# Kernel tuning notes

Measured on AMD Instinct MI355X. Metric: run time of the kernel, lower is better.

The kernel has to match this reference:

```python
import jax, jax.numpy as jnp
import numpy as np

N_NODES = 100000
N_EDGES = 1600000


def setup_inputs() -> dict:
    key = jax.random.key(0)
    ks = jax.random.split(key, 12)
    s = lambda d: 1.0 / np.sqrt(d)
    inp = {
        "x": jax.random.normal(ks[0], (N_NODES, 64), dtype=jnp.float32),
        "edge_index": jax.random.randint(ks[1], (2, N_EDGES), 0, N_NODES, dtype=jnp.int64),
        "W_embed": jax.random.normal(ks[2], (64, 128), dtype=jnp.float32) * s(64),
        "eps1": jnp.zeros((), jnp.float32),
        "w1a": jax.random.normal(ks[3], (128, 128), dtype=jnp.float32) * s(128),
        "b1a": jnp.zeros((128,), jnp.float32),
        "w1b": jax.random.normal(ks[4], (128, 128), dtype=jnp.float32) * s(128),
        "b1b": jnp.zeros((128,), jnp.float32),
        "eps2": jnp.zeros((), jnp.float32),
        "w2a": jax.random.normal(ks[5], (128, 256), dtype=jnp.float32) * s(128),
        "b2a": jnp.zeros((256,), jnp.float32),
        "w2b": jax.random.normal(ks[6], (256, 128), dtype=jnp.float32) * s(256),
        "b2b": jnp.zeros((128,), jnp.float32),
        "eps3": jnp.zeros((), jnp.float32),
        "w3a": jax.random.normal(ks[7], (128, 256), dtype=jnp.float32) * s(128),
        "b3a": jnp.zeros((256,), jnp.float32),
        "w3b": jax.random.normal(ks[8], (256, 128), dtype=jnp.float32) * s(256),
        "b3b": jnp.zeros((128,), jnp.float32),
    }
    return inp


def _aggregate(h, src, dst, n):
    # GINConv sum aggregation: out[i] = sum_{(j,i) in E} h[j]
    return jax.ops.segment_sum(h[src], dst, num_segments=n)


def reference(x, edge_index, W_embed, eps1, w1a, b1a, w1b, b1b,
              eps2, w2a, b2a, w2b, b2b, eps3, w3a, b3a, w3b, b3b):
    src, dst = edge_index[0], edge_index[1]
    n = x.shape[0]
    # node_attr_encoder: linear embedding (dropout p=0 -> identity)
    h = x @ W_embed  # [N, dim]
    # conv1: nn((1+eps)*h + sum_neighbors), nn = Lin->ReLU->Lin
    z = (1.0 + eps1) * h + _aggregate(h, src, dst, n)
    h = jax.nn.relu(z @ w1a + b1a) @ w1b + b1b
    # conv2/conv3: nn = Lin->ReLU->Lin->ReLU
    z = (1.0 + eps2) * h + _aggregate(h, src, dst, n)
    h = jax.nn.relu(jax.nn.relu(z @ w2a + b2a) @ w2b + b2b)
    z = (1.0 + eps3) * h + _aggregate(h, src, dst, n)
    h = jax.nn.relu(jax.nn.relu(z @ w3a + b3a) @ w3b + b3b)
    return h
```

## Files before the change

### kernel.cpp

```cpp
#include <hip/hip_runtime.h>
#include <hip/hip_bf16.h>
#include <stdint.h>


typedef __attribute__((ext_vector_type(8))) short short8;
typedef __attribute__((ext_vector_type(16))) float float16v;
typedef __attribute__((ext_vector_type(4))) unsigned int uint4v;

#define BKT 512
#define NBMAX 256

#define MFMA32 __builtin_amdgcn_mfma_f32_32x32x16_bf16

union U4S8 { uint4v u; short8 s; };

__device__ __forceinline__ float b2f_lo(unsigned int u) {
    return __uint_as_float(u << 16);
}
__device__ __forceinline__ float b2f_hi(unsigned int u) {
    return __uint_as_float(u & 0xffff0000u);
}
__device__ __forceinline__ unsigned short f2b(float f) {
    unsigned int u = __float_as_uint(f);
    return (unsigned short)((u + 0x7fffu + ((u >> 16) & 1u)) >> 16);
}
__device__ __forceinline__ unsigned cvtpk_bf16(float a, float b) {
    unsigned r;
    asm("v_cvt_pk_bf16_f32 %0, %1, %2" : "=v"(r) : "v"(a), "v"(b));
    return r;
}
__device__ __forceinline__ void perm32swap(unsigned& a, unsigned& b) {
    asm("v_permlane32_swap_b32 %0, %1" : "+v"(a), "+v"(b));
}

__global__ void detect_i64_kernel(const unsigned int* ei, int* flag) {
    if (threadIdx.x == 0) {
        int is64 = 1;
        for (int e = 0; e < 64; ++e)
            if (ei[2 * e + 1] != 0u) { is64 = 0; break; }
        *flag = is64;
    }
}

__device__ __forceinline__ int edge_at(const int* ei32, int is64, long long pos) {
    if (is64) return (int)(((const long long*)ei32)[pos]);
    return ei32[pos];
}

__global__ __launch_bounds__(256) void part_hist_kernel(
        const int* __restrict__ ei, const int* __restrict__ flag,
        int* __restrict__ bh, int E, int NB, int PB) {
    __shared__ int h[NBMAX];
    const int g = blockIdx.x, tid = threadIdx.x;
    const int is64 = *flag;
    for (int i = tid; i < NB; i += 256) h[i] = 0;
    __syncthreads();
    const int e0 = g * PB, e1 = min(e0 + PB, E);
    for (int e = e0 + tid; e < e1; e += 256) {
        int d = edge_at(ei, is64, (long long)E + e);
        atomicAdd(&h[d >> 9], 1);
    }
    __syncthreads();
    for (int i = tid; i < NB; i += 256) bh[i * gridDim.x + g] = h[i];
}

__global__ __launch_bounds__(1024) void scan1_kernel(
        const int* __restrict__ in, int* __restrict__ out,
        int* __restrict__ partial, int n) {
    __shared__ int sm[1024];
    const int t = threadIdx.x;
    const int i = blockIdx.x * 1024 + t;
    int v = (i < n) ? in[i] : 0;
    sm[t] = v;
    __syncthreads();
#pragma unroll
    for (int off = 1; off < 1024; off <<= 1) {
        int x = (t >= off) ? sm[t - off] : 0;
        __syncthreads();
        sm[t] += x;
        __syncthreads();
    }
    if (i < n) out[i] = sm[t] - v;
    if (t == 1023) partial[blockIdx.x] = sm[1023];
}

__global__ __launch_bounds__(256) void scan2_kernel(
        int* __restrict__ partial, int* __restrict__ blockoff, int g1) {
    __shared__ int sm[256];
    const int t = threadIdx.x;
    int v = (t < g1) ? partial[t] : 0;
    sm[t] = v;
    __syncthreads();
#pragma unroll
    for (int off = 1; off < 256; off <<= 1) {
        int x = (t >= off) ? sm[t - off] : 0;
        __syncthreads();
        sm[t] += x;
        __syncthreads();
    }
    blockoff[t] = sm[t] - v;
}

__global__ __launch_bounds__(1024) void scan3g_kernel(
        int* __restrict__ a, const int* __restrict__ blockoff, int n) {
    int i = blockIdx.x * 1024 + threadIdx.x;
    if (i < n) a[i] += blockoff[blockIdx.x];
}

__global__ __launch_bounds__(256) void part_scatter_kernel(
        const int* __restrict__ ei, const int* __restrict__ flag,
        const int* __restrict__ bhs, unsigned int* __restrict__ staged,
        int E, int NB, int PB) {
    __shared__ int cur[NBMAX];
    const int g = blockIdx.x, tid = threadIdx.x;
    const int is64 = *flag;
    for (int i = tid; i < NB; i += 256) cur[i] = bhs[i * gridDim.x + g];
    __syncthreads();
    const int e0 = g * PB, e1 = min(e0 + PB, E);
    for (int e = e0 + tid; e < e1; e += 256) {
        int d = edge_at(ei, is64, (long long)E + e);
        int s = edge_at(ei, is64, (long long)e);
        int b = d >> 9;
        int p = atomicAdd(&cur[b], 1);
        staged[p] = ((unsigned int)(d & (BKT - 1)) << 17) | (unsigned int)s;
    }
}

__global__ __launch_bounds__(256) void csr_local_kernel(
        const unsigned int* __restrict__ staged, const int* __restrict__ bhs,
        int* __restrict__ offs, int* __restrict__ csr, int N, int E, int NB, int G2) {
    __shared__ int hist[BKT];
    __shared__ int cur[BKT];
    const int b = blockIdx.x;
    const int tid = threadIdx.x;
    const int start = bhs[b * G2];
    const int end = (b + 1 < NB) ? bhs[(b + 1) * G2] : E;
    const int node0 = b * BKT;
    for (int i = tid; i < BKT; i += 256) hist[i] = 0;
    __syncthreads();
    for (int i = start + tid; i < end; i += 256)
        atomicAdd(&hist[staged[i] >> 17], 1);
    __syncthreads();
    const int i0 = tid * 2, i1 = i0 + 1;
    for (int off = 1; off < BKT; off <<= 1) {
        int v0 = (i0 >= off) ? hist[i0 - off] : 0;
        int v1 = (i1 >= off) ? hist[i1 - off] : 0;
        __syncthreads();
        hist[i0] += v0;
        hist[i1] += v1;
        __syncthreads();
    }
    for (int i = tid; i < BKT; i += 256) {
        int node = node0 + i;
        if (node < N) {
            int e0 = start + ((i == 0) ? 0 : hist[i - 1]);
            offs[node] = e0;
            cur[i] = e0;
        }
    }
    if (b == NB - 1 && tid == 0) offs[N] = E;
    __syncthreads();
    for (int i = start + tid; i < end; i += 256) {
        unsigned int v = staged[i];
        int dl = v >> 17;
        int src = (int)(v & 0x1ffff);
        int p = atomicAdd(&cur[dl], 1);
        csr[p] = src;
    }
}

struct PW { const float* W; unsigned short* o; int K; int KOUT; };
struct PWAll { PW d[7]; int cum[8]; };

__global__ __launch_bounds__(256) void packall_kernel(PWAll P) {
    int id = blockIdx.x * blockDim.x + threadIdx.x;
    if (id >= P.cum[7]) return;
    int w = 0;
#pragma unroll
    for (int k = 1; k < 7; ++k) w += (id >= P.cum[k]);
    const int local = id - P.cum[w];
    const float* W = P.d[w].W;
    unsigned short* out = P.d[w].o;
    const int K = P.d[w].K, KOUT = P.d[w].KOUT;
    const int KS = K / 16;
    const int l = local & 63;
    const int s = (local >> 6) % KS;
    const int T = local / (KS * 64);
    const int kbase = s * 16 + ((l >> 5) << 3);
    const int n = T * 32 + (l & 31);
#pragma unroll
    for (int j = 0; j < 8; ++j)
        out[(long long)local * 8 + j] = f2b(W[(long long)(kbase + j) * KOUT + n]);
}

__global__ __launch_bounds__(256) void mm_embed(
        const float* __restrict__ X, const unsigned short* __restrict__ Wp,
        unsigned short* __restrict__ out, int Mreal) {
    constexpr int KS = 4;
    const int tid = threadIdx.x;
    const int w = tid >> 6;
    const int l = tid & 63;
    const int lm = l & 31;
    const int lk = l >> 5;
    const int wr = w & 1, wc = w >> 1;
    const long long R0 = (long long)blockIdx.x * 128 + wr * 64;
    const int T0 = (wc * 64) >> 5;

    const long long r0 = (R0 + lm < Mreal) ? (R0 + lm) : (Mreal - 1);
    const long long r1 = (R0 + 32 + lm < Mreal) ? (R0 + 32 + lm) : (Mreal - 1);
    const float* xr0 = X + r0 * 64 + lk * 8;
    const float* xr1 = X + r1 * 64 + lk * 8;
    const unsigned short* bb0 = Wp + ((long long)T0 * KS * 64 + l) * 8;
    const unsigned short* bb1 = Wp + ((long long)(T0 + 1) * KS * 64 + l) * 8;

    float16v acc00 = {}, acc01 = {}, acc10 = {}, acc11 = {};
#pragma unroll
    for (int s = 0; s < KS; ++s) {
        float4 f0a = *(const float4*)(xr0 + s * 16);
        float4 f0b = *(const float4*)(xr0 + s * 16 + 4);
        float4 f1a = *(const float4*)(xr1 + s * 16);
        float4 f1b = *(const float4*)(xr1 + s * 16 + 4);
        short8 a0, a1;
        a0[0] = (short)f2b(f0a.x); a0[1] = (short)f2b(f0a.y);
        a0[2] = (short)f2b(f0a.z); a0[3] = (short)f2b(f0a.w);
        a0[4] = (short)f2b(f0b.x); a0[5] = (short)f2b(f0b.y);
        a0[6] = (short)f2b(f0b.z); a0[7] = (short)f2b(f0b.w);
        a1[0] = (short)f2b(f1a.x); a1[1] = (short)f2b(f1a.y);
        a1[2] = (short)f2b(f1a.z); a1[3] = (short)f2b(f1a.w);
        a1[4] = (short)f2b(f1b.x); a1[5] = (short)f2b(f1b.y);
        a1[6] = (short)f2b(f1b.z); a1[7] = (short)f2b(f1b.w);
        short8 b0 = *(const short8*)(bb0 + (long long)s * 64 * 8);
        short8 b1 = *(const short8*)(bb1 + (long long)s * 64 * 8);
        acc00 = MFMA32(a0, b0, acc00, 0, 0, 0);
        acc01 = MFMA32(a0, b1, acc01, 0, 0, 0);
        acc10 = MFMA32(a1, b0, acc10, 0, 0, 0);
        acc11 = MFMA32(a1, b1, acc11, 0, 0, 0);
    }
    auto st = [&](float16v acc, long long rb, int col) {
#pragma unroll
        for (int r = 0; r < 16; ++r) {
            long long row = rb + (r & 3) + 8 * (r >> 2);
            out[row * 128 + col] = f2b(acc[r]);
        }
    };
    const long long rbase = R0 + 4 * lk;
    st(acc00, rbase,      wc * 64 + lm);
    st(acc01, rbase,      wc * 64 + 32 + lm);
    st(acc10, rbase + 32, wc * 64 + lm);
    st(acc11, rbase + 32, wc * 64 + 32 + lm);
}

__global__ __launch_bounds__(256) void aggz_kernel(
        const unsigned short* __restrict__ H, const int* __restrict__ offs,
        const int* __restrict__ csr, const float* __restrict__ eps,
        unsigned short* __restrict__ Z, int n) {
    const int node = blockIdx.x * 16 + (threadIdx.x >> 4);
    const int c8 = (threadIdx.x & 15) << 3;
    const int lane = threadIdx.x & 63;
    const int bpb = (lane & 48) << 2;
    const int g16 = threadIdx.x & 15;
    if (node >= n) return;
    const int beg = offs[node];
    const int end = offs[node + 1];
    const unsigned short* Hc = H + c8;
    const uint4 uh = *(const uint4*)(Hc + ((long long)node << 7));
    float a0 = 0.f, a1 = 0.f, a2 = 0.f, a3 = 0.f;
    float a4 = 0.f, a5 = 0.f, a6 = 0.f, a7 = 0.f;
    int i = beg;
    for (; i + 8 <= end; i += 8) {
        const int myidx = csr[i + (g16 & 7)];
        const int s0 = __builtin_amdgcn_ds_bpermute(bpb + 0,  myidx);
        const int s1 = __builtin_amdgcn_ds_bpermute(bpb + 4,  myidx);
        const int s2 = __builtin_amdgcn_ds_bpermute(bpb + 8,  myidx);
        const int s3 = __builtin_amdgcn_ds_bpermute(bpb + 12, myidx);
        const int s4 = __builtin_amdgcn_ds_bpermute(bpb + 16, myidx);
        const int s5 = __builtin_amdgcn_ds_bpermute(bpb + 20, myidx);
        const int s6 = __builtin_amdgcn_ds_bpermute(bpb + 24, myidx);
        const int s7 = __builtin_amdgcn_ds_bpermute(bpb + 28, myidx);
        const uint4 u0 = *(const uint4*)(Hc + ((long long)s0 << 7));
        const uint4 u1 = *(const uint4*)(Hc + ((long long)s1 << 7));
        const uint4 u2 = *(const uint4*)(Hc + ((long long)s2 << 7));
        const uint4 u3 = *(const uint4*)(Hc + ((long long)s3 << 7));
        const uint4 u4 = *(const uint4*)(Hc + ((long long)s4 << 7));
        const uint4 u5 = *(const uint4*)(Hc + ((long long)s5 << 7));
        const uint4 u6 = *(const uint4*)(Hc + ((long long)s6 << 7));
        const uint4 u7 = *(const uint4*)(Hc + ((long long)s7 << 7));
        a0 += ((b2f_lo(u0.x) + b2f_lo(u1.x)) + (b2f_lo(u2.x) + b2f_lo(u3.x)))
            + ((b2f_lo(u4.x) + b2f_lo(u5.x)) + (b2f_lo(u6.x) + b2f_lo(u7.x)));
        a1 += ((b2f_hi(u0.x) + b2f_hi(u1.x)) + (b2f_hi(u2.x) + b2f_hi(u3.x)))
            + ((b2f_hi(u4.x) + b2f_hi(u5.x)) + (b2f_hi(u6.x) + b2f_hi(u7.x)));
        a2 += ((b2f_lo(u0.y) + b2f_lo(u1.y)) + (b2f_lo(u2.y) + b2f_lo(u3.y)))
            + ((b2f_lo(u4.y) + b2f_lo(u5.y)) + (b2f_lo(u6.y) + b2f_lo(u7.y)));
        a3 += ((b2f_hi(u0.y) + b2f_hi(u1.y)) + (b2f_hi(u2.y) + b2f_hi(u3.y)))
            + ((b2f_hi(u4.y) + b2f_hi(u5.y)) + (b2f_hi(u6.y) + b2f_hi(u7.y)));
        a4 += ((b2f_lo(u0.z) + b2f_lo(u1.z)) + (b2f_lo(u2.z) + b2f_lo(u3.z)))
            + ((b2f_lo(u4.z) + b2f_lo(u5.z)) + (b2f_lo(u6.z) + b2f_lo(u7.z)));
        a5 += ((b2f_hi(u0.z) + b2f_hi(u1.z)) + (b2f_hi(u2.z) + b2f_hi(u3.z)))
            + ((b2f_hi(u4.z) + b2f_hi(u5.z)) + (b2f_hi(u6.z) + b2f_hi(u7.z)));
        a6 += ((b2f_lo(u0.w) + b2f_lo(u1.w)) + (b2f_lo(u2.w) + b2f_lo(u3.w)))
            + ((b2f_lo(u4.w) + b2f_lo(u5.w)) + (b2f_lo(u6.w) + b2f_lo(u7.w)));
        a7 += ((b2f_hi(u0.w) + b2f_hi(u1.w)) + (b2f_hi(u2.w) + b2f_hi(u3.w)))
            + ((b2f_hi(u4.w) + b2f_hi(u5.w)) + (b2f_hi(u6.w) + b2f_hi(u7.w)));
    }
    for (; i + 3 < end; i += 4) {
        const int j0 = csr[i], j1 = csr[i + 1], j2 = csr[i + 2], j3 = csr[i + 3];
        const uint4 u0 = *(const uint4*)(Hc + ((long long)j0 << 7));
        const uint4 u1 = *(const uint4*)(Hc + ((long long)j1 << 7));
        const uint4 u2 = *(const uint4*)(Hc + ((long long)j2 << 7));
        const uint4 u3 = *(const uint4*)(Hc + ((long long)j3 << 7));
        a0 += (b2f_lo(u0.x) + b2f_lo(u1.x)) + (b2f_lo(u2.x) + b2f_lo(u3.x));
        a1 += (b2f_hi(u0.x) + b2f_hi(u1.x)) + (b2f_hi(u2.x) + b2f_hi(u3.x));
        a2 += (b2f_lo(u0.y) + b2f_lo(u1.y)) + (b2f_lo(u2.y) + b2f_lo(u3.y));
        a3 += (b2f_hi(u0.y) + b2f_hi(u1.y)) + (b2f_hi(u2.y) + b2f_hi(u3.y));
        a4 += (b2f_lo(u0.z) + b2f_lo(u1.z)) + (b2f_lo(u2.z) + b2f_lo(u3.z));
        a5 += (b2f_hi(u0.z) + b2f_hi(u1.z)) + (b2f_hi(u2.z) + b2f_hi(u3.z));
        a6 += (b2f_lo(u0.w) + b2f_lo(u1.w)) + (b2f_lo(u2.w) + b2f_lo(u3.w));
        a7 += (b2f_hi(u0.w) + b2f_hi(u1.w)) + (b2f_hi(u2.w) + b2f_hi(u3.w));
    }
    for (; i < end; ++i) {
        const uint4 u0 = *(const uint4*)(Hc + ((long long)csr[i] << 7));
        a0 += b2f_lo(u0.x); a1 += b2f_hi(u0.x);
        a2 += b2f_lo(u0.y); a3 += b2f_hi(u0.y);
        a4 += b2f_lo(u0.z); a5 += b2f_hi(u0.z);
        a6 += b2f_lo(u0.w); a7 += b2f_hi(u0.w);
    }
    const float e = 1.0f + eps[0];
    a0 = fmaf(e, b2f_lo(uh.x), a0); a1 = fmaf(e, b2f_hi(uh.x), a1);
    a2 = fmaf(e, b2f_lo(uh.y), a2); a3 = fmaf(e, b2f_hi(uh.y), a3);
    a4 = fmaf(e, b2f_lo(uh.z), a4); a5 = fmaf(e, b2f_hi(uh.z), a5);
    a6 = fmaf(e, b2f_lo(uh.w), a6); a7 = fmaf(e, b2f_hi(uh.w), a7);
    uint4 o;
    o.x = ((unsigned int)f2b(a1) << 16) | (unsigned int)f2b(a0);
    o.y = ((unsigned int)f2b(a3) << 16) | (unsigned int)f2b(a2);
    o.z = ((unsigned int)f2b(a5) << 16) | (unsigned int)f2b(a4);
    o.w = ((unsigned int)f2b(a7) << 16) | (unsigned int)f2b(a6);
    *(uint4*)(Z + ((long long)node << 7) + c8) = o;
}


#define CVT_TO_PA2(ACC, P0, P1) do {                                   \
        unsigned X1 = cvtpk_bf16((ACC)[0], (ACC)[1]);                  \
        unsigned Y1 = cvtpk_bf16((ACC)[4], (ACC)[5]);                  \
        unsigned X2 = cvtpk_bf16((ACC)[2], (ACC)[3]);                  \
        unsigned Y2 = cvtpk_bf16((ACC)[6], (ACC)[7]);                  \
        perm32swap(X1, Y1); perm32swap(X2, Y2);                        \
        U4S8 u0; u0.u[0] = X1; u0.u[1] = X2; u0.u[2] = Y1; u0.u[3] = Y2; \
        (P0) = u0.s;                                                   \
        unsigned X3 = cvtpk_bf16((ACC)[8], (ACC)[9]);                  \
        unsigned Y3 = cvtpk_bf16((ACC)[12], (ACC)[13]);                \
        unsigned X4 = cvtpk_bf16((ACC)[10], (ACC)[11]);                \
        unsigned Y4 = cvtpk_bf16((ACC)[14], (ACC)[15]);                \
        perm32swap(X3, Y3); perm32swap(X4, Y4);                        \
        U4S8 u1; u1.u[0] = X3; u1.u[1] = X4; u1.u[2] = Y3; u1.u[3] = Y4; \
        (P1) = u1.s;                                                   \
    } while (0)

template<int KMID, bool RELU2, bool OUTF32>
__global__ __launch_bounds__(512, 2) void fused_mlp3(
        const unsigned short* __restrict__ Zin,
        const unsigned short* __restrict__ Wap, const float* __restrict__ ba,
        const unsigned short* __restrict__ Wbp, const float* __restrict__ bb,
        void* __restrict__ outp, int Mreal, int nstrips) {
    constexpr int NF = KMID / 32;
    constexpr int NCH = KMID / 16;
    constexpr int WAS = 128 * KMID;
    __shared__ unsigned short wlds[KMID * 256];
    __shared__ float blds[KMID + 128];
    const int tid = threadIdx.x;

    {
        const uint4* sa = (const uint4*)Wap;
        const uint4* sb = (const uint4*)Wbp;
        uint4* da = (uint4*)wlds;
        uint4* db = (uint4*)(wlds + WAS);
#pragma unroll
        for (int i = tid; i < KMID * 16; i += 512) { da[i] = sa[i]; db[i] = sb[i]; }
        for (int i = tid; i < KMID; i += 512) blds[i] = ba[i];
        if (tid < 128) blds[KMID + tid] = bb[tid];
    }
    __syncthreads();

    const int wid = tid >> 6;
    const int l = tid & 63;
    const int lo = l & 31;
    const int hi = l >> 5;
    const int stride = gridDim.x * 8;
    int strip = blockIdx.x * 8 + wid;
    if (strip >= nstrips) return;

    auto zload = [&](int s_, short8* zz) {
        long long zr = (long long)s_ * 32 + lo;
        if (zr >= Mreal) zr = Mreal - 1;
        const unsigned short* zrow = Zin + zr * 128 + hi * 8;
#pragma unroll
        for (int s = 0; s < 8; ++s) zz[s] = *(const short8*)(zrow + s * 16);
    };

    short8 zc[8];
    zload(strip, zc);

    while (strip < nstrips) {
        const int nxt = strip + stride;
        float16v acc2[4] = {};
        short8 zn[8];

#pragma unroll
        for (int fp = 0; fp < NF / 2; ++fp) {
            if (fp == NF / 2 - 1) {
                if (nxt < nstrips) zload(nxt, zn);
            }
            const int f0 = 2 * fp, f1 = f0 + 1;
            float16v accA, accB;
#pragma unroll
            for (int q = 0; q < 4; ++q) {
                const float4 tA = *(const float4*)(blds + f0 * 32 + q * 8 + hi * 4);
                const float4 tB = *(const float4*)(blds + f1 * 32 + q * 8 + hi * 4);
                accA[4 * q + 0] = tA.x; accA[4 * q + 1] = tA.y;
                accA[4 * q + 2] = tA.z; accA[4 * q + 3] = tA.w;
                accB[4 * q + 0] = tB.x; accB[4 * q + 1] = tB.y;
                accB[4 * q + 2] = tB.z; accB[4 * q + 3] = tB.w;
            }
            const unsigned short* wa0 = wlds + ((long long)(f0 * 8) * 64 + l) * 8;
            const unsigned short* wa1 = wlds + ((long long)(f1 * 8) * 64 + l) * 8;
#pragma unroll
            for (int s = 0; s < 8; ++s) {
                short8 a0 = *(const short8*)(wa0 + s * 64 * 8);
                short8 a1 = *(const short8*)(wa1 + s * 64 * 8);
                accA = MFMA32(a0, zc[s], accA, 0, 0, 0);
                accB = MFMA32(a1, zc[s], accB, 0, 0, 0);
            }
#pragma unroll
            for (int r = 0; r < 16; ++r) {
                accA[r] = fmaxf(accA[r], 0.f);
                accB[r] = fmaxf(accB[r], 0.f);
            }
            short8 pa0, pa1, pa2, pa3;
            CVT_TO_PA2(accA, pa0, pa1);
            CVT_TO_PA2(accB, pa2, pa3);
            const unsigned short* wb = wlds + WAS + ((long long)(fp * 4) * 64 + l) * 8;
#pragma unroll
            for (int g = 0; g < 4; ++g) {
                const unsigned short* wbg = wb + (long long)g * NCH * 64 * 8;
                short8 b0 = *(const short8*)(wbg);
                short8 b1 = *(const short8*)(wbg + 64 * 8);
                short8 b2 = *(const short8*)(wbg + 2 * 64 * 8);
                short8 b3 = *(const short8*)(wbg + 3 * 64 * 8);
                acc2[g] = MFMA32(pa0, b0, acc2[g], 0, 0, 0);
                acc2[g] = MFMA32(pa1, b1, acc2[g], 0, 0, 0);
                acc2[g] = MFMA32(pa2, b2, acc2[g], 0, 0, 0);
                acc2[g] = MFMA32(pa3, b3, acc2[g], 0, 0, 0);
            }
        }

#pragma unroll
        for (int g = 0; g < 4; ++g) {
            const int col = g * 32 + lo;
            const float bv = blds[KMID + col];
#pragma unroll
            for (int r = 0; r < 16; ++r) {
                float v = acc2[g][r] + bv;
                if (RELU2) v = fmaxf(v, 0.f);
                const long long node = (long long)strip * 32 + (r & 3) + 8 * (r >> 2) + 4 * hi;
                if (node < Mreal) {
                    if (OUTF32) ((float*)outp)[node * 128 + col] = v;
                    else ((unsigned short*)outp)[node * 128 + col] = f2b(v);
                }
            }
        }

        strip = nxt;
        if (strip < nstrips) {
#pragma unroll
            for (int s = 0; s < 8; ++s) zc[s] = zn[s];
        }
    }
}

extern "C" void kernel_launch(void* const* d_in, const int* in_sizes, int n_in,
                              void* d_out, int out_size, void* d_ws, size_t ws_size,
                              hipStream_t stream) {
    const float* x    = (const float*)d_in[0];
    const int*   ei   = (const int*)d_in[1];
    const float* Wemb = (const float*)d_in[2];
    const float* eps1 = (const float*)d_in[3];
    const float* w1a  = (const float*)d_in[4];
    const float* b1a  = (const float*)d_in[5];
    const float* w1b  = (const float*)d_in[6];
    const float* b1b  = (const float*)d_in[7];
    const float* eps2 = (const float*)d_in[8];
    const float* w2a  = (const float*)d_in[9];
    const float* b2a  = (const float*)d_in[10];
    const float* w2b  = (const float*)d_in[11];
    const float* b2b  = (const float*)d_in[12];
    const float* eps3 = (const float*)d_in[13];
    const float* w3a  = (const float*)d_in[14];
    const float* b3a  = (const float*)d_in[15];
    const float* w3b  = (const float*)d_in[16];
    const float* b3b  = (const float*)d_in[17];

    const int N = in_sizes[0] / 64;
    const int E = in_sizes[1] / 2;
    const int Mpad = ((N + 127) / 128) * 128;
    const int NB = (N + BKT - 1) / BKT;
    const int G2 = 1024;
    const int PB = (E + G2 - 1) / G2;
    const int BH = NB * G2;

    char* ws = (char*)d_ws;
    size_t off = 0;
    auto alloc = [&](size_t bytes) -> void* {
        void* p = ws + off;
        off = (off + bytes + 255) & ~(size_t)255;
        return p;
    };
    unsigned short* Ha  = (unsigned short*)alloc((size_t)Mpad * 128 * 2);
    unsigned short* Hb2 = (unsigned short*)alloc((size_t)Mpad * 128 * 2);
    unsigned short* Zb  = (unsigned short*)alloc((size_t)Mpad * 128 * 2);
    unsigned short* pWe = (unsigned short*)alloc((size_t)64 * 128 * 2);
    unsigned short* p1a = (unsigned short*)alloc((size_t)128 * 128 * 2);
    unsigned short* p1b = (unsigned short*)alloc((size_t)128 * 128 * 2);
    unsigned short* p2a = (unsigned short*)alloc((size_t)128 * 256 * 2);
    unsigned short* p2b = (unsigned short*)alloc((size_t)256 * 128 * 2);
    unsigned short* p3a = (unsigned short*)alloc((size_t)128 * 256 * 2);
    unsigned short* p3b = (unsigned short*)alloc((size_t)256 * 128 * 2);
    int* offs = (int*)alloc((size_t)(N + 1) * 4);
    int* csr  = (int*)alloc((size_t)E * 4);
    unsigned int* staged = (unsigned int*)alloc((size_t)E * 4);
    int* bh   = (int*)alloc((size_t)BH * 4);
    int* bhs  = (int*)alloc((size_t)BH * 4);
    int* part = (int*)alloc(1024);
    int* boff = (int*)alloc(1024);
    int* flag = (int*)alloc(256);

    detect_i64_kernel<<<1, 64, 0, stream>>>((const unsigned int*)ei, flag);
    part_hist_kernel<<<G2, 256, 0, stream>>>(ei, flag, bh, E, NB, PB);
    const int G1 = (BH + 1023) / 1024;
    scan1_kernel<<<G1, 1024, 0, stream>>>(bh, bhs, part, BH);
    scan2_kernel<<<1, 256, 0, stream>>>(part, boff, G1);
    scan3g_kernel<<<G1, 1024, 0, stream>>>(bhs, boff, BH);
    part_scatter_kernel<<<G2, 256, 0, stream>>>(ei, flag, bhs, staged, E, NB, PB);
    csr_local_kernel<<<NB, 256, 0, stream>>>(staged, bhs, offs, csr, N, E, NB, G2);

    {
        PWAll P;
        const PW descs[7] = {
            {Wemb, pWe, 64, 128}, {w1a, p1a, 128, 128}, {w1b, p1b, 128, 128},
            {w2a, p2a, 128, 256}, {w2b, p2b, 256, 128}, {w3a, p3a, 128, 256},
            {w3b, p3b, 256, 128}};
        int c = 0;
        for (int k = 0; k < 7; ++k) {
            P.d[k] = descs[k];
            P.cum[k] = c;
            c += (descs[k].KOUT / 32) * (descs[k].K / 16) * 64;
        }
        P.cum[7] = c;
        packall_kernel<<<(c + 255) / 256, 256, 0, stream>>>(P);
    }

    const int MMB = Mpad / 128;
    const int AGB = (N + 15) / 16;
    const int NSTRIP = (N + 31) / 32;
    const int MLPG = 256;

    mm_embed<<<MMB, 256, 0, stream>>>(x, pWe, Ha, N);

    aggz_kernel<<<AGB, 256, 0, stream>>>(Ha, offs, csr, eps1, Zb, N);
    fused_mlp3<128, false, false><<<MLPG, 512, 0, stream>>>(Zb, p1a, b1a, p1b, b1b, Hb2, N, NSTRIP);

    aggz_kernel<<<AGB, 256, 0, stream>>>(Hb2, offs, csr, eps2, Zb, N);
    fused_mlp3<256, true, false><<<MLPG, 512, 0, stream>>>(Zb, p2a, b2a, p2b, b2b, Ha, N, NSTRIP);

    aggz_kernel<<<AGB, 256, 0, stream>>>(Ha, offs, csr, eps3, Zb, N);
    fused_mlp3<256, true, true><<<MLPG, 512, 0, stream>>>(Zb, p3a, b3a, p3b, b3b, d_out, N, NSTRIP);
}
```

Before: 444.4 us.

## Raise MLP block to 12 waves, drop Z prefetch, split second GEMM to cut registers

The fused MLP kernel now runs 768-thread blocks (12 waves per block) with launch bounds targeting 3 blocks per CU instead of 512 threads and 2 blocks. The software prefetch of the next strip's Z rows is removed, and the second-layer MFMAs are split into two halves so only two packed activation fragments are live at a time. Both changes lower register pressure so more waves fit, letting the extra waves hide load latency in place of explicit prefetching. The risk is exposed global-load latency if occupancy does not actually rise, and LDS use (up to 128KB of weights per block for KMID=256) may not allow three blocks per CU.

```diff
diff --git a/kernel.cpp b/kernel.cpp
--- a/kernel.cpp
+++ b/kernel.cpp
@@ -356,7 +356,7 @@
     } while (0)
 
 template<int KMID, bool RELU2, bool OUTF32>
-__global__ __launch_bounds__(512, 2) void fused_mlp3(
+__global__ __launch_bounds__(768, 3) void fused_mlp4(
         const unsigned short* __restrict__ Zin,
         const unsigned short* __restrict__ Wap, const float* __restrict__ ba,
         const unsigned short* __restrict__ Wbp, const float* __restrict__ bb,
@@ -373,9 +373,8 @@
         const uint4* sb = (const uint4*)Wbp;
         uint4* da = (uint4*)wlds;
         uint4* db = (uint4*)(wlds + WAS);
-#pragma unroll
-        for (int i = tid; i < KMID * 16; i += 512) { da[i] = sa[i]; db[i] = sb[i]; }
-        for (int i = tid; i < KMID; i += 512) blds[i] = ba[i];
+        for (int i = tid; i < KMID * 16; i += 768) { da[i] = sa[i]; db[i] = sb[i]; }
+        for (int i = tid; i < KMID; i += 768) blds[i] = ba[i];
         if (tid < 128) blds[KMID + tid] = bb[tid];
     }
     __syncthreads();
@@ -384,31 +383,22 @@
     const int l = tid & 63;
     const int lo = l & 31;
     const int hi = l >> 5;
-    const int stride = gridDim.x * 8;
-    int strip = blockIdx.x * 8 + wid;
-    if (strip >= nstrips) return;
-
-    auto zload = [&](int s_, short8* zz) {
-        long long zr = (long long)s_ * 32 + lo;
+    const int stride = gridDim.x * 12;
+
+    for (int strip = blockIdx.x * 12 + wid; strip < nstrips; strip += stride) {
+        const long long node0 = (long long)strip * 32;
+
+        long long zr = node0 + lo;
         if (zr >= Mreal) zr = Mreal - 1;
         const unsigned short* zrow = Zin + zr * 128 + hi * 8;
-#pragma unroll
-        for (int s = 0; s < 8; ++s) zz[s] = *(const short8*)(zrow + s * 16);
-    };
-
-    short8 zc[8];
-    zload(strip, zc);
-
-    while (strip < nstrips) {
-        const int nxt = strip + stride;
+        short8 zc[8];
+#pragma unroll
+        for (int s = 0; s < 8; ++s) zc[s] = *(const short8*)(zrow + s * 16);
+
         float16v acc2[4] = {};
-        short8 zn[8];
 
 #pragma unroll
         for (int fp = 0; fp < NF / 2; ++fp) {
-            if (fp == NF / 2 - 1) {
-                if (nxt < nstrips) zload(nxt, zn);
-            }
             const int f0 = 2 * fp, f1 = f0 + 1;
             float16v accA, accB;
 #pragma unroll
@@ -434,21 +424,30 @@
                 accA[r] = fmaxf(accA[r], 0.f);
                 accB[r] = fmaxf(accB[r], 0.f);
             }
-            short8 pa0, pa1, pa2, pa3;
-            CVT_TO_PA2(accA, pa0, pa1);
-            CVT_TO_PA2(accB, pa2, pa3);
             const unsigned short* wb = wlds + WAS + ((long long)(fp * 4) * 64 + l) * 8;
-#pragma unroll
-            for (int g = 0; g < 4; ++g) {
-                const unsigned short* wbg = wb + (long long)g * NCH * 64 * 8;
-                short8 b0 = *(const short8*)(wbg);
-                short8 b1 = *(const short8*)(wbg + 64 * 8);
-                short8 b2 = *(const short8*)(wbg + 2 * 64 * 8);
-                short8 b3 = *(const short8*)(wbg + 3 * 64 * 8);
-                acc2[g] = MFMA32(pa0, b0, acc2[g], 0, 0, 0);
-                acc2[g] = MFMA32(pa1, b1, acc2[g], 0, 0, 0);
-                acc2[g] = MFMA32(pa2, b2, acc2[g], 0, 0, 0);
-                acc2[g] = MFMA32(pa3, b3, acc2[g], 0, 0, 0);
+            {
+                short8 pa0, pa1;
+                CVT_TO_PA2(accA, pa0, pa1);
+#pragma unroll
+                for (int g = 0; g < 4; ++g) {
+                    const unsigned short* wbg = wb + (long long)g * NCH * 64 * 8;
+                    short8 b0 = *(const short8*)(wbg);
+                    short8 b1 = *(const short8*)(wbg + 64 * 8);
+                    acc2[g] = MFMA32(pa0, b0, acc2[g], 0, 0, 0);
+                    acc2[g] = MFMA32(pa1, b1, acc2[g], 0, 0, 0);
+                }
+            }
+            {
+                short8 pa2, pa3;
+                CVT_TO_PA2(accB, pa2, pa3);
+#pragma unroll
+                for (int g = 0; g < 4; ++g) {
+                    const unsigned short* wbg = wb + (long long)g * NCH * 64 * 8;
+                    short8 b2 = *(const short8*)(wbg + 2 * 64 * 8);
+                    short8 b3 = *(const short8*)(wbg + 3 * 64 * 8);
+                    acc2[g] = MFMA32(pa2, b2, acc2[g], 0, 0, 0);
+                    acc2[g] = MFMA32(pa3, b3, acc2[g], 0, 0, 0);
+                }
             }
         }
 
@@ -460,18 +459,12 @@
             for (int r = 0; r < 16; ++r) {
                 float v = acc2[g][r] + bv;
                 if (RELU2) v = fmaxf(v, 0.f);
-                const long long node = (long long)strip * 32 + (r & 3) + 8 * (r >> 2) + 4 * hi;
+                const long long node = node0 + (r & 3) + 8 * (r >> 2) + 4 * hi;
                 if (node < Mreal) {
                     if (OUTF32) ((float*)outp)[node * 128 + col] = v;
                     else ((unsigned short*)outp)[node * 128 + col] = f2b(v);
                 }
             }
-        }
-
-        strip = nxt;
-        if (strip < nstrips) {
-#pragma unroll
-            for (int s = 0; s < 8; ++s) zc[s] = zn[s];
         }
     }
 }
@@ -565,11 +558,11 @@
     mm_embed<<<MMB, 256, 0, stream>>>(x, pWe, Ha, N);
 
     aggz_kernel<<<AGB, 256, 0, stream>>>(Ha, offs, csr, eps1, Zb, N);
-    fused_mlp3<128, false, false><<<MLPG, 512, 0, stream>>>(Zb, p1a, b1a, p1b, b1b, Hb2, N, NSTRIP);
+    fused_mlp4<128, false, false><<<MLPG, 768, 0, stream>>>(Zb, p1a, b1a, p1b, b1b, Hb2, N, NSTRIP);
 
     aggz_kernel<<<AGB, 256, 0, stream>>>(Hb2, offs, csr, eps2, Zb, N);
-    fused_mlp3<256, true, false><<<MLPG, 512, 0, stream>>>(Zb, p2a, b2a, p2b, b2b, Ha, N, NSTRIP);
+    fused_mlp4<256, true, false><<<MLPG, 768, 0, stream>>>(Zb, p2a, b2a, p2b, b2b, Ha, N, NSTRIP);
 
     aggz_kernel<<<AGB, 256, 0, stream>>>(Ha, offs, csr, eps3, Zb, N);
-    fused_mlp3<256, true, true><<<MLPG, 512, 0, stream>>>(Zb, p3a, b3a, p3b, b3b, d_out, N, NSTRIP);
-}
+    fused_mlp4<256, true, true><<<MLPG, 768, 0, stream>>>(Zb, p3a, b3a, p3b, b3b, d_out, N, NSTRIP);
+}
```

After: 522.1 us. 17.5% more time.
